# Optimization experiments

Measured on AMD Instinct MI355X. Metric: run time of the kernel, lower is better.

## Reference

```python
import jax, jax.numpy as jnp
import numpy as np

D = 8192          # dimension (high_dim_mode since > 1000)
M = 1_600_000     # ~0.05 * D*(D-1) pairs after the i>j mask
RIEMANN_SHIFT = 0.5


def _lower_tri_pairs(rng, d, m):
    # Sample m unique strictly-lower-triangular (i, j) positions (i > j).
    total = d * (d - 1) // 2
    k = rng.choice(total, size=m, replace=False)
    kf = k.astype(np.float64)
    i = np.floor((1.0 + np.sqrt(1.0 + 8.0 * kf)) / 2.0).astype(np.int64)
    # fix possible off-by-one from float sqrt
    tri = i * (i - 1) // 2
    i = np.where(tri > k, i - 1, i)
    tri = i * (i - 1) // 2
    j = k - tri
    return i, j


def setup_inputs() -> dict:
    key = jax.random.key(0)
    k1, k2 = jax.random.split(key)
    rng = np.random.default_rng(0)

    i, j = _lower_tri_pairs(rng, D, M)
    interaction_indices = jnp.asarray(np.stack([i, j]))  # [2, M] int64

    local_scale = 1.0 / D ** 0.75
    h_local = jax.random.normal(k1, (D,), dtype=jnp.float32) * local_scale + RIEMANN_SHIFT

    dim_factor = 1.0 / (D ** 0.9 * np.log(D))
    V_interaction = jax.random.normal(k2, (M,), dtype=jnp.float32) * dim_factor

    return {
        "h_local": h_local,
        "V_interaction": V_interaction,
        "interaction_indices": interaction_indices,
        "dimension": D,
    }


def reference(h_local, V_interaction, interaction_indices, dimension) -> jnp.ndarray:
    d = h_local.shape[0]
    # scatter interaction values into strict lower triangle (set semantics,
    # indices are unique so set == torch assignment)
    H_int = jnp.zeros((d, d), dtype=h_local.dtype)
    H_int = H_int.at[interaction_indices[0], interaction_indices[1]].set(V_interaction)
    H_int = H_int + H_int.T  # symmetrize
    interaction_scale = 1.0 - 0.2 / np.sqrt(np.log(dimension))
    return jnp.diag(h_local) + H_int * interaction_scale
```

## Files before the change

### kernel.cpp

```cpp
#include <hip/hip_runtime.h>
#include <math.h>


#define P1_PAIRS 2048
#define NBKT     512
#define BCAP     16
#define SENTK    0xFFFFFFFFu
#define OVFCAP   65536


__global__ __launch_bounds__(64) void zero_hdr_kernel(int* __restrict__ hdr)
{
    if (threadIdx.x == 0) hdr[0] = 0;
}

__global__ __launch_bounds__(512) void p1_kernel(
    const int*   __restrict__ idx,
    const float* __restrict__ vals,
    float scale, int m, int nblk,
    uint2* __restrict__ region1,
    uint2* __restrict__ ovf,
    int*   __restrict__ hdr)
{
    __shared__ uint2 stage[NBKT][BCAP];
    __shared__ int   cnt[NBKT];

    for (int f = threadIdx.x; f < NBKT * BCAP; f += 512)
        stage[f >> 4][f & 15] = make_uint2(SENTK, 0u);
    for (int b = threadIdx.x; b < NBKT; b += 512) cnt[b] = 0;
    __syncthreads();

    const int blk  = blockIdx.x;
    const int base = blk * P1_PAIRS;
#pragma unroll
    for (int it = 0; it < P1_PAIRS / 512; ++it) {
        int k = base + it * 512 + threadIdx.x;
        if (k < m) {
            int i = idx[k];
            int j = idx[m + k];
            unsigned vb = __float_as_uint(vals[k] * scale);

            unsigned k1 = ((unsigned)i << 13) | (unsigned)j;
            int b1 = i >> 4;
            int p = atomicAdd(&cnt[b1], 1);
            if (p < BCAP) stage[b1][p] = make_uint2(k1, vb);
            else { int q = atomicAdd(hdr, 1); if (q < OVFCAP) ovf[q] = make_uint2(k1, vb); }

            unsigned k2 = ((unsigned)j << 13) | (unsigned)i;
            int b2 = j >> 4;
            p = atomicAdd(&cnt[b2], 1);
            if (p < BCAP) stage[b2][p] = make_uint2(k2, vb);
            else { int q = atomicAdd(hdr, 1); if (q < OVFCAP) ovf[q] = make_uint2(k2, vb); }
        }
    }
    __syncthreads();

    for (int f = threadIdx.x; f < NBKT * BCAP; f += 512) {
        int b = f >> 4, e = f & 15;
        region1[((long long)b * nblk + blk) * BCAP + e] = stage[b][e];
    }
}

__global__ __launch_bounds__(512) void p2_kernel(
    float* __restrict__ out,
    const float* __restrict__ h_local,
    const uint2* __restrict__ region1,
    int nblk,
    const uint2* __restrict__ ovf,
    const int*   __restrict__ hdr)
{
    __shared__ float srow[4 * 8192];
    float4* s4 = reinterpret_cast<float4*>(srow);
    const int band = blockIdx.x;
    const int g    = band >> 2;

    for (int c = threadIdx.x; c < 8192; c += 512)
        s4[c] = make_float4(0.f, 0.f, 0.f, 0.f);
    __syncthreads();

    const uint4* src = reinterpret_cast<const uint4*>(
        region1 + (long long)g * nblk * BCAP);
    const int n2 = (nblk * BCAP) >> 1;
    const unsigned bandu = (unsigned)band;
    for (int e = threadIdx.x; e < n2; e += 512) {
        uint4 en = src[e];
        if ((en.x >> 15) == bandu) srow[en.x & 0x7FFF] = __uint_as_float(en.y);
        if ((en.z >> 15) == bandu) srow[en.z & 0x7FFF] = __uint_as_float(en.w);
    }
    int n = hdr[0]; if (n > OVFCAP) n = OVFCAP;
    for (int e = threadIdx.x; e < n; e += 512) {
        uint2 en = ovf[e];
        if ((en.x >> 15) == bandu) srow[en.x & 0x7FFF] = __uint_as_float(en.y);
    }
    if (threadIdx.x < 4) {
        int r = (band << 2) + threadIdx.x;
        srow[((unsigned)threadIdx.x << 13) | (unsigned)r] = h_local[r];
    }
    __syncthreads();

    float4* orow = reinterpret_cast<float4*>(out + ((long long)band << 15));
    for (int c = threadIdx.x; c < 8192; c += 512)
        orow[c] = s4[c];
}


__global__ __launch_bounds__(256) void init_counts_kernel(
    float* __restrict__ out, int d, int logd)
{
    int r = blockIdx.x * blockDim.x + threadIdx.x;
    if (r < d) reinterpret_cast<int*>(out)[(long long)r << logd] = 0;
}

__global__ __launch_bounds__(256) void bin_kernel(
    float* __restrict__ out,
    const int*   __restrict__ idx,
    const float* __restrict__ vals,
    float scale, int m, int logd, int cap)
{
    int k = blockIdx.x * blockDim.x + threadIdx.x;
    if (k >= m) return;
    int i = idx[k];
    int j = idx[m + k];
    unsigned vb = __float_as_uint(vals[k] * scale);
    int* cnt_i = reinterpret_cast<int*>(out) + ((long long)i << logd);
    int* cnt_j = reinterpret_cast<int*>(out) + ((long long)j << logd);
    int p1 = atomicAdd(cnt_i, 1);
    if (p1 < cap)
        *reinterpret_cast<uint2*>(out + ((long long)i << logd) + 2 + 2 * p1) =
            make_uint2((unsigned)j, vb);
    int p2 = atomicAdd(cnt_j, 1);
    if (p2 < cap)
        *reinterpret_cast<uint2*>(out + ((long long)j << logd) + 2 + 2 * p2) =
            make_uint2((unsigned)i, vb);
}

__global__ __launch_bounds__(256) void rows_kernel(
    float* __restrict__ out,
    const float* __restrict__ h_local,
    int logd, int cap)
{
    __shared__ float srow[8192];
    const int d  = 1 << logd;
    const int n4 = d >> 2;
    float4* s4 = reinterpret_cast<float4*>(srow);
    const int r = blockIdx.x;
    float* grow = out + ((long long)r << logd);
    const float4 z = make_float4(0.f, 0.f, 0.f, 0.f);
    for (int c = threadIdx.x; c < n4; c += blockDim.x) s4[c] = z;
    __syncthreads();
    int cnt = reinterpret_cast<const int*>(grow)[0];
    if (cnt > cap) cnt = cap;
    const uint2* eb = reinterpret_cast<const uint2*>(grow + 2);
    for (int e = threadIdx.x; e < cnt; e += blockDim.x) {
        uint2 p = eb[e];
        srow[p.x] = __uint_as_float(p.y);
    }
    if (threadIdx.x == 0) srow[r] = h_local[r];
    __syncthreads();
    for (int c = threadIdx.x; c < n4; c += blockDim.x)
        reinterpret_cast<float4*>(grow)[c] = s4[c];
}

__global__ __launch_bounds__(256) void fill_diag_kernel(
    float* __restrict__ out, const float* __restrict__ h_local,
    int d, long long n)
{
    long long t = (long long)blockIdx.x * blockDim.x + threadIdx.x;
    if (t >= n) return;
    long long row = t / d;
    long long col = t - row * d;
    out[t] = (row == col) ? h_local[row] : 0.f;
}

__global__ __launch_bounds__(256) void scatter_kernel(
    float* __restrict__ out,
    const int* __restrict__ idx,
    const float* __restrict__ vals,
    float scale, int m, int d)
{
    int k = blockIdx.x * blockDim.x + threadIdx.x;
    if (k >= m) return;
    int i = idx[k];
    int j = idx[m + k];
    float v = vals[k] * scale;
    out[(long long)i * d + j] = v;
    out[(long long)j * d + i] = v;
}


extern "C" void kernel_launch(void* const* d_in, const int* in_sizes, int n_in,
                              void* d_out, int out_size, void* d_ws, size_t ws_size,
                              hipStream_t stream) {
    const float* h_local = (const float*)d_in[0];
    const float* V_int   = (const float*)d_in[1];
    const int*   idx     = (const int*)d_in[2];

    const int d = in_sizes[0];
    const int m = in_sizes[1];

    int logd = 0;
    while ((1 << logd) < d) ++logd;
    const bool pow2 = ((1 << logd) == d);

    const float iscale = (float)(1.0 - 0.2 / sqrt(log((double)d)));
    float* out = (float*)d_out;
    const int block = 256;

    const int nblk = (m + P1_PAIRS - 1) / P1_PAIRS;

    const size_t off_ovf = 4096;
    const size_t off_r1  = off_ovf + (size_t)OVFCAP * sizeof(uint2);
    const size_t ws_need = off_r1 + (size_t)NBKT * nblk * BCAP * sizeof(uint2);

    const bool path5 = (d == 8192) && (m > 0) && (m <= 3000000) &&
                       (d_ws != nullptr) && (ws_size >= ws_need);

    if (path5) {
        char* ws = (char*)d_ws;
        int*   hdr     = (int*)ws;
        uint2* ovf     = (uint2*)(ws + off_ovf);
        uint2* region1 = (uint2*)(ws + off_r1);

        zero_hdr_kernel<<<1, 64, 0, stream>>>(hdr);
        p1_kernel<<<nblk, 512, 0, stream>>>(idx, V_int, iscale, m, nblk,
                                            region1, ovf, hdr);
        p2_kernel<<<2048, 512, 0, stream>>>(out, h_local, region1, nblk, ovf, hdr);
    } else if (pow2 && d >= 1024 && d <= 8192 &&
               ((long long)m * 2 / d) < (long long)((d - 2) / 2) / 2) {
        const int cap = (d - 2) / 2;
        init_counts_kernel<<<(d + block - 1) / block, block, 0, stream>>>(out, d, logd);
        bin_kernel<<<(m + block - 1) / block, block, 0, stream>>>(out, idx, V_int,
                                                                  iscale, m, logd, cap);
        rows_kernel<<<d, block, 0, stream>>>(out, h_local, logd, cap);
    } else {
        const long long n = (long long)d * d;
        const long long grid_fill = (n + block - 1) / block;
        fill_diag_kernel<<<(dim3)(unsigned)grid_fill, block, 0, stream>>>(out, h_local, d, n);
        const int grid_sc = (m + block - 1) / block;
        scatter_kernel<<<grid_sc, block, 0, stream>>>(out, idx, V_int, iscale, m, d);
    }
}
```

Baseline: 370.6 us.

## Bin pairs directly by 4-row band and scatter overflow in a separate pass

Phase 1 now bins each pair into one of 2048 buckets keyed by its 4-row band, with 8 slots per bucket, so each phase-2 block reads only entries belonging to its own band and no longer filters out the three quarters of entries meant for other bands. Overflow entries go into a per-block shared-memory list that is written out per block, with a global list as the last fallback. A new kernel scatters all overflow entries straight into the output after the dense band write. This removes redundant region reads and the full global overflow scan that every band block did before. The cost is an extra launch, more sentinel traffic from the larger bucket count, and heavier overflow from the small buckets.

Result: faster. 320.4 us (-13.6%).

```diff
diff --git a/kernel.cpp b/kernel.cpp
--- a/kernel.cpp
+++ b/kernel.cpp
@@ -2,95 +2,105 @@
 #include <math.h>
 
 
-#define P1_PAIRS 2048
-#define NBKT     512
-#define BCAP     16
+#define P1_PAIRS 4096
+#define NBKT     2048
+#define BCAP     8
+#define OVB      512
 #define SENTK    0xFFFFFFFFu
-#define OVFCAP   65536
-
-
-__global__ __launch_bounds__(64) void zero_hdr_kernel(int* __restrict__ hdr)
-{
-    if (threadIdx.x == 0) hdr[0] = 0;
-}
-
-__global__ __launch_bounds__(512) void p1_kernel(
+#define GCAP     65536
+
+
+__global__ __launch_bounds__(64) void zero_hdr_kernel(int* __restrict__ ghdr)
+{
+    if (threadIdx.x == 0) ghdr[0] = 0;
+}
+
+__global__ __launch_bounds__(1024) void p1_kernel(
     const int*   __restrict__ idx,
     const float* __restrict__ vals,
     float scale, int m, int nblk,
     uint2* __restrict__ region1,
     uint2* __restrict__ ovf,
-    int*   __restrict__ hdr)
+    int*   __restrict__ ovfc,
+    uint2* __restrict__ glist,
+    int*   __restrict__ ghdr)
 {
     __shared__ uint2 stage[NBKT][BCAP];
     __shared__ int   cnt[NBKT];
-
-    for (int f = threadIdx.x; f < NBKT * BCAP; f += 512)
-        stage[f >> 4][f & 15] = make_uint2(SENTK, 0u);
-    for (int b = threadIdx.x; b < NBKT; b += 512) cnt[b] = 0;
+    __shared__ uint2 ovfst[OVB];
+    __shared__ int   ovfn;
+
+    uint2* sflat = &stage[0][0];
+    for (int f = threadIdx.x; f < NBKT * BCAP; f += 1024)
+        sflat[f] = make_uint2(SENTK, 0u);
+    for (int b = threadIdx.x; b < NBKT; b += 1024) cnt[b] = 0;
+    if (threadIdx.x == 0) ovfn = 0;
     __syncthreads();
 
     const int blk  = blockIdx.x;
     const int base = blk * P1_PAIRS;
 #pragma unroll
-    for (int it = 0; it < P1_PAIRS / 512; ++it) {
-        int k = base + it * 512 + threadIdx.x;
+    for (int it = 0; it < P1_PAIRS / 1024; ++it) {
+        int k = base + it * 1024 + threadIdx.x;
         if (k < m) {
             int i = idx[k];
             int j = idx[m + k];
             unsigned vb = __float_as_uint(vals[k] * scale);
 
             unsigned k1 = ((unsigned)i << 13) | (unsigned)j;
-            int b1 = i >> 4;
+            int b1 = i >> 2;
             int p = atomicAdd(&cnt[b1], 1);
             if (p < BCAP) stage[b1][p] = make_uint2(k1, vb);
-            else { int q = atomicAdd(hdr, 1); if (q < OVFCAP) ovf[q] = make_uint2(k1, vb); }
+            else {
+                int q = atomicAdd(&ovfn, 1);
+                if (q < OVB) ovfst[q] = make_uint2(k1, vb);
+                else { int g = atomicAdd(ghdr, 1); if (g < GCAP) glist[g] = make_uint2(k1, vb); }
+            }
 
             unsigned k2 = ((unsigned)j << 13) | (unsigned)i;
-            int b2 = j >> 4;
+            int b2 = j >> 2;
             p = atomicAdd(&cnt[b2], 1);
             if (p < BCAP) stage[b2][p] = make_uint2(k2, vb);
-            else { int q = atomicAdd(hdr, 1); if (q < OVFCAP) ovf[q] = make_uint2(k2, vb); }
+            else {
+                int q = atomicAdd(&ovfn, 1);
+                if (q < OVB) ovfst[q] = make_uint2(k2, vb);
+                else { int g = atomicAdd(ghdr, 1); if (g < GCAP) glist[g] = make_uint2(k2, vb); }
+            }
         }
     }
     __syncthreads();
 
-    for (int f = threadIdx.x; f < NBKT * BCAP; f += 512) {
-        int b = f >> 4, e = f & 15;
-        region1[((long long)b * nblk + blk) * BCAP + e] = stage[b][e];
-    }
-}
-
-__global__ __launch_bounds__(512) void p2_kernel(
+    for (int f = threadIdx.x; f < NBKT * BCAP; f += 1024) {
+        int b = f >> 3, e = f & 7;
+        region1[((long long)b * nblk + blk) * BCAP + e] = sflat[f];
+    }
+    int n = ovfn; if (n > OVB) n = OVB;
+    for (int e = threadIdx.x; e < n; e += 1024)
+        ovf[(long long)blk * OVB + e] = ovfst[e];
+    if (threadIdx.x == 0) ovfc[blk] = n;
+}
+
+__global__ __launch_bounds__(1024) void p2_kernel(
     float* __restrict__ out,
     const float* __restrict__ h_local,
     const uint2* __restrict__ region1,
-    int nblk,
-    const uint2* __restrict__ ovf,
-    const int*   __restrict__ hdr)
+    int nblk)
 {
     __shared__ float srow[4 * 8192];
     float4* s4 = reinterpret_cast<float4*>(srow);
     const int band = blockIdx.x;
-    const int g    = band >> 2;
-
-    for (int c = threadIdx.x; c < 8192; c += 512)
+
+    for (int c = threadIdx.x; c < 8192; c += 1024)
         s4[c] = make_float4(0.f, 0.f, 0.f, 0.f);
     __syncthreads();
 
     const uint4* src = reinterpret_cast<const uint4*>(
-        region1 + (long long)g * nblk * BCAP);
+        region1 + (long long)band * nblk * BCAP);
     const int n2 = (nblk * BCAP) >> 1;
-    const unsigned bandu = (unsigned)band;
-    for (int e = threadIdx.x; e < n2; e += 512) {
+    for (int e = threadIdx.x; e < n2; e += 1024) {
         uint4 en = src[e];
-        if ((en.x >> 15) == bandu) srow[en.x & 0x7FFF] = __uint_as_float(en.y);
-        if ((en.z >> 15) == bandu) srow[en.z & 0x7FFF] = __uint_as_float(en.w);
-    }
-    int n = hdr[0]; if (n > OVFCAP) n = OVFCAP;
-    for (int e = threadIdx.x; e < n; e += 512) {
-        uint2 en = ovf[e];
-        if ((en.x >> 15) == bandu) srow[en.x & 0x7FFF] = __uint_as_float(en.y);
+        if (en.x != SENTK) srow[en.x & 0x7FFF] = __uint_as_float(en.y);
+        if (en.z != SENTK) srow[en.z & 0x7FFF] = __uint_as_float(en.w);
     }
     if (threadIdx.x < 4) {
         int r = (band << 2) + threadIdx.x;
@@ -99,8 +109,30 @@
     __syncthreads();
 
     float4* orow = reinterpret_cast<float4*>(out + ((long long)band << 15));
-    for (int c = threadIdx.x; c < 8192; c += 512)
+    for (int c = threadIdx.x; c < 8192; c += 1024)
         orow[c] = s4[c];
+}
+
+__global__ __launch_bounds__(256) void ovf_scatter_kernel(
+    float* __restrict__ out,
+    const uint2* __restrict__ ovf,
+    const int*   __restrict__ ovfc,
+    const uint2* __restrict__ glist,
+    const int*   __restrict__ ghdr)
+{
+    const int blk = blockIdx.x;
+    int n = ovfc[blk]; if (n > OVB) n = OVB;
+    for (int e = threadIdx.x; e < n; e += 256) {
+        uint2 en = ovf[(long long)blk * OVB + e];
+        out[en.x] = __uint_as_float(en.y);
+    }
+    if (blk == 0) {
+        int g = ghdr[0]; if (g > GCAP) g = GCAP;
+        for (int e = threadIdx.x; e < g; e += 256) {
+            uint2 en = glist[e];
+            out[en.x] = __uint_as_float(en.y);
+        }
+    }
 }
 
 
@@ -208,23 +240,29 @@
 
     const int nblk = (m + P1_PAIRS - 1) / P1_PAIRS;
 
-    const size_t off_ovf = 4096;
-    const size_t off_r1  = off_ovf + (size_t)OVFCAP * sizeof(uint2);
-    const size_t ws_need = off_r1 + (size_t)NBKT * nblk * BCAP * sizeof(uint2);
-
-    const bool path5 = (d == 8192) && (m > 0) && (m <= 3000000) &&
+    const size_t off_ovfc  = 4096;
+    const size_t off_glist = off_ovfc + (((size_t)nblk * 4 + 4095) & ~(size_t)4095);
+    const size_t off_ovf   = off_glist + (size_t)GCAP * sizeof(uint2);
+    const size_t off_r1    = off_ovf + (((size_t)nblk * OVB * sizeof(uint2) + 4095)
+                                        & ~(size_t)4095);
+    const size_t ws_need   = off_r1 + (size_t)NBKT * nblk * BCAP * sizeof(uint2);
+
+    const bool path6 = (d == 8192) && (m > 0) && (m <= 2000000) &&
                        (d_ws != nullptr) && (ws_size >= ws_need);
 
-    if (path5) {
+    if (path6) {
         char* ws = (char*)d_ws;
-        int*   hdr     = (int*)ws;
+        int*   ghdr    = (int*)ws;
+        int*   ovfc    = (int*)(ws + off_ovfc);
+        uint2* glist   = (uint2*)(ws + off_glist);
         uint2* ovf     = (uint2*)(ws + off_ovf);
         uint2* region1 = (uint2*)(ws + off_r1);
 
-        zero_hdr_kernel<<<1, 64, 0, stream>>>(hdr);
-        p1_kernel<<<nblk, 512, 0, stream>>>(idx, V_int, iscale, m, nblk,
-                                            region1, ovf, hdr);
-        p2_kernel<<<2048, 512, 0, stream>>>(out, h_local, region1, nblk, ovf, hdr);
+        zero_hdr_kernel<<<1, 64, 0, stream>>>(ghdr);
+        p1_kernel<<<nblk, 1024, 0, stream>>>(idx, V_int, iscale, m, nblk,
+                                             region1, ovf, ovfc, glist, ghdr);
+        p2_kernel<<<NBKT, 1024, 0, stream>>>(out, h_local, region1, nblk);
+        ovf_scatter_kernel<<<nblk, 256, 0, stream>>>(out, ovf, ovfc, glist, ghdr);
     } else if (pow2 && d >= 1024 && d <= 8192 &&
                ((long long)m * 2 / d) < (long long)((d - 2) / 2) / 2) {
         const int cap = (d - 2) / 2;
```
